# Kernel tuning notes

Hardware: AMD Instinct MI355X
Metric: run time of the kernel (lower is better)

The kernel has to match this reference:

```python
import jax, jax.numpy as jnp
import numpy as np

N, D = 16384, 16     # nodes (hits), node feature dim (= embedding dim, slice is full)
K = 64               # max_num_neighbors
MAX_RADIUS = 6.0     # kNN radius cut
PID_MAX = 5000


def setup_inputs() -> dict:
    key = jax.random.key(0)
    k1, k2 = jax.random.split(key)
    x = jax.random.normal(k1, (N, D), dtype=jnp.float32)
    particle_id = jax.random.randint(k2, (N,), 0, PID_MAX, dtype=jnp.int32)
    return {"x": x, "particle_id": particle_id}


def reference(x, particle_id):
    # ml is None and embedding_slice=(None,None) -> embedding features are x itself
    emb = x
    # knn_graph: squared pairwise distances, self-loops excluded (diag = +inf)
    sq = jnp.sum(emb * emb, axis=1)                       # [N]
    d2 = sq[:, None] + sq[None, :] - 2.0 * (emb @ emb.T)  # [N, N]
    diag = jnp.arange(N)
    d2 = d2.at[diag, diag].set(jnp.inf)
    _, nbr = jax.lax.top_k(-d2, K)                        # [N, K] nearest neighbor ids
    src = nbr.reshape(-1)                                 # edge_index[0]: neighbor (source)
    dst = jnp.repeat(jnp.arange(N, dtype=src.dtype), K)   # edge_index[1]: query node
    # radius filter: keep edges with dist < max_radius (fixed shape -> boolean mask)
    diff = x[src] - x[dst]                                # [N*K, D]
    dists = jnp.sqrt(jnp.maximum(jnp.sum(diff * diff, axis=1), 0.0))
    mask = dists < MAX_RADIUS                             # [N*K]
    # edge truth labels: same (nonzero) particle id on both ends
    y = (particle_id[src] == particle_id[dst]) & (particle_id[src] > 0) & mask
    # edge features: [x_src - x_dst, x_src + x_dst], zeroed on masked-out edges
    edge_features = jnp.concatenate([diff, x[src] + x[dst]], axis=1)
    edge_features = edge_features * mask[:, None].astype(x.dtype)
    edge_index = jnp.stack([src, dst])                    # [2, N*K]
    return x, edge_index, y.astype(jnp.int32), edge_features, mask
```

## Files before the change

kernel.cpp:

```cpp
#include <hip/hip_runtime.h>
#include <hip/hip_fp16.h>

#define NN 16384
#define DD 16
#define KK 64
#define QQ 4
#define TPB 256
#define NQW 16
#define HIST 1024
#define HISTW (HIST/2)
#define LIST_MAX 768
#define CAND_MAX 256
#define EPS 1.5f

__device__ __forceinline__ float halving_sumsq16(const float* v) {
    float p[16];
#pragma unroll
    for (int d = 0; d < 16; ++d) p[d] = __fmul_rn(v[d], v[d]);
    float r8[8];
#pragma unroll
    for (int j = 0; j < 8; ++j) r8[j] = __fadd_rn(p[j], p[j + 8]);
    float r4[4];
#pragma unroll
    for (int j = 0; j < 4; ++j) r4[j] = __fadd_rn(r8[j], r8[j + 4]);
    float r2[2];
#pragma unroll
    for (int j = 0; j < 2; ++j) r2[j] = __fadd_rn(r4[j], r4[j + 2]);
    return __fadd_rn(r2[0], r2[1]);
}

__device__ __forceinline__ float d2_of(const float* xi, const float* xj,
                                       float sqi, float sqj) {
    float dot = 0.0f;
#pragma unroll
    for (int d = 0; d < DD; ++d) dot = fmaf(xi[d], xj[d], dot);
    return __fsub_rn(__fadd_rn(sqi, sqj), __fmul_rn(2.0f, dot));
}

__device__ __forceinline__ int bucket_of(float d2) {
    int b = (int)__fmul_rn(d2, 4.0f);
    if (b < 0) b = 0;
    if (b >= HIST) b = HIST - 1;
    return b;
}

__device__ __forceinline__ float tq_of(float s) {
    return 16.0f + s - 2.0f * sqrtf(32.0f + 4.0f * s);
}

#define LOAD_XQ()                                                              \
    float xq[QQ][DD];                                                          \
    float sq[QQ], Tq[QQ];                                                      \
    _Pragma("unroll") for (int q = 0; q < QQ; ++q) {                           \
        const float4* p = reinterpret_cast<const float4*>(x + (iA + q) * DD);  \
        float4 a0 = p[0], a1 = p[1], a2 = p[2], a3 = p[3];                     \
        xq[q][0]=a0.x; xq[q][1]=a0.y; xq[q][2]=a0.z; xq[q][3]=a0.w;            \
        xq[q][4]=a1.x; xq[q][5]=a1.y; xq[q][6]=a1.z; xq[q][7]=a1.w;            \
        xq[q][8]=a2.x; xq[q][9]=a2.y; xq[q][10]=a2.z; xq[q][11]=a2.w;          \
        xq[q][12]=a3.x; xq[q][13]=a3.y; xq[q][14]=a3.z; xq[q][15]=a3.w;        \
        sq[q] = sqf[iA + q];                                                   \
        Tq[q] = tq_of(sq[q]);                                                  \
    }

#define LOAD_XJ(j)                                                             \
    const float4* xj4 = reinterpret_cast<const float4*>(x + (j) * DD);         \
    float4 a0 = xj4[0], a1 = xj4[1], a2 = xj4[2], a3 = xj4[3];                 \
    float xj[DD] = {a0.x, a0.y, a0.z, a0.w, a1.x, a1.y, a1.z, a1.w,            \
                    a2.x, a2.y, a2.z, a2.w, a3.x, a3.y, a3.z, a3.w};

__global__ void prep_kernel(const float* __restrict__ x,
                            float* __restrict__ out_x,
                            float* __restrict__ sqf,
                            __half* __restrict__ xh) {
    int i = blockIdx.x * blockDim.x + threadIdx.x;
    if (i < NN) {
        float v[DD];
#pragma unroll
        for (int d = 0; d < DD; ++d) v[d] = x[i * DD + d];
        sqf[i] = halving_sumsq16(v);
#pragma unroll
        for (int p = 0; p < 8; ++p) {
            xh[((long)p * NN + i) * 2 + 0] = __float2half(v[2 * p]);
            xh[((long)p * NN + i) * 2 + 1] = __float2half(v[2 * p + 1]);
        }
    }
    for (int t = i; t < NN * DD; t += gridDim.x * blockDim.x) {
        out_x[t] = x[t];
    }
}

__global__ __launch_bounds__(TPB, 4) void scan_kernel(
        const __half2* __restrict__ xh2,
        const float* __restrict__ sqf,
        unsigned int* __restrict__ ws_cnt,
        unsigned short* __restrict__ ws_list) {
    __shared__ unsigned short bm[NQW][TPB];
    __shared__ unsigned short list[QQ][LIST_MAX];
    __shared__ unsigned int wcnt[TPB / 64][QQ];
    __shared__ unsigned int s_listcnt[QQ];

    const int tid = threadIdx.x;
    const int lane = tid & 63;
    const int w = tid >> 6;
    const int iA = blockIdx.x * QQ;

    __half2 qh[QQ][8];
    float Cq[QQ];
#pragma unroll
    for (int q = 0; q < QQ; ++q) {
        const float* xr = (const float*)sqf;
    }
#pragma unroll
    for (int q = 0; q < QQ; ++q)
#pragma unroll
        for (int p = 0; p < 8; ++p)
            qh[q][p] = xh2[(long)p * NN + (iA + q)];
#pragma unroll
    for (int q = 0; q < QQ; ++q) {
        float s = sqf[iA + q];
        Cq[q] = 0.5f * (s - tq_of(s) - EPS);
    }

#pragma unroll 1
    for (int c = 0; c < NQW; ++c) {
        const int qd = c * TPB + tid;
        float4 sjv = reinterpret_cast<const float4*>(sqf)[qd];
        __half2 acc[QQ][4];
#pragma unroll
        for (int q = 0; q < QQ; ++q)
#pragma unroll
            for (int jl = 0; jl < 4; ++jl)
                acc[q][jl] = __half2(__float2half(0.f), __float2half(0.f));
#pragma unroll
        for (int p = 0; p < 8; ++p) {
            const __half2* hp = &xh2[(long)p * NN + 4 * (long)qd];
            __half2 h0 = hp[0], h1 = hp[1], h2 = hp[2], h3 = hp[3];
#pragma unroll
            for (int q = 0; q < QQ; ++q) {
                acc[q][0] = __hfma2(qh[q][p], h0, acc[q][0]);
                acc[q][1] = __hfma2(qh[q][p], h1, acc[q][1]);
                acc[q][2] = __hfma2(qh[q][p], h2, acc[q][2]);
                acc[q][3] = __hfma2(qh[q][p], h3, acc[q][3]);
            }
        }
        unsigned int bits = 0;
        float sjq[4] = {sjv.x, sjv.y, sjv.z, sjv.w};
#pragma unroll
        for (int jl = 0; jl < 4; ++jl) {
#pragma unroll
            for (int q = 0; q < QQ; ++q) {
                float dot = __low2float(acc[q][jl]) + __high2float(acc[q][jl]);
                float thr = fmaf(sjq[jl], 0.5f, Cq[q]);
                if (dot > thr) bits |= (1u << (jl * 4 + q));
            }
        }
        bm[c][tid] = (unsigned short)bits;
    }
    __syncthreads();

    {
        unsigned int cnt[QQ] = {0, 0, 0, 0};
#pragma unroll 1
        for (int c = 0; c < NQW; ++c) {
            unsigned int w16 = bm[c][tid];
#pragma unroll
            for (int q = 0; q < QQ; ++q)
                cnt[q] += (unsigned int)__popc(w16 & (0x1111u << q));
        }
        unsigned int excl[QQ];
#pragma unroll
        for (int q = 0; q < QQ; ++q) {
            unsigned int v = cnt[q];
#pragma unroll
            for (int off = 1; off < 64; off <<= 1) {
                unsigned int n = __shfl_up(v, off, 64);
                if (lane >= off) v += n;
            }
            excl[q] = v - cnt[q];
            if (lane == 63) wcnt[w][q] = v;
        }
        __syncthreads();
        if (tid < QQ)
            s_listcnt[tid] = wcnt[0][tid] + wcnt[1][tid] + wcnt[2][tid] + wcnt[3][tid];
        unsigned int cur[QQ];
#pragma unroll
        for (int q = 0; q < QQ; ++q) {
            unsigned int b = 0;
            for (int ww = 0; ww < w; ++ww) b += wcnt[ww][q];
            cur[q] = b + excl[q];
        }
#pragma unroll 1
        for (int c = 0; c < NQW; ++c) {
            unsigned int t16 = bm[c][tid];
            while (t16) {
                int b = __ffs(t16) - 1;
                int q = b & 3;
                int jl = b >> 2;
                unsigned int pos = cur[q]++;
                if (pos < LIST_MAX)
                    list[q][pos] = (unsigned short)((c * TPB + tid) * 4 + jl);
                t16 &= t16 - 1;
            }
        }
    }
    __syncthreads();

    for (int q = 0; q < QQ; ++q) {
        int lc = (int)min(s_listcnt[q], (unsigned int)LIST_MAX);
        unsigned short* dst = ws_list + ((long)iA + q) * LIST_MAX;
        for (int e = tid; e < lc; e += TPB) dst[e] = list[q][e];
    }
    if (tid < QQ) ws_cnt[iA + tid] = s_listcnt[tid];
}

__global__ __launch_bounds__(TPB) void select_kernel(
        const float* __restrict__ x,
        const int* __restrict__ pid,
        const float* __restrict__ sqf,
        const unsigned int* __restrict__ ws_cnt,
        const unsigned short* __restrict__ ws_list,
        float* __restrict__ out_src,
        float* __restrict__ out_dst,
        float* __restrict__ out_y,
        float* __restrict__ out_ef,
        float* __restrict__ out_mask) {
    __shared__ unsigned short list[QQ][LIST_MAX];
    __shared__ unsigned int hist[QQ][HISTW];
    __shared__ unsigned int cand_key[QQ][CAND_MAX];
    __shared__ int cand_idx[QQ][CAND_MAX];
    __shared__ unsigned int wavesum[QQ][TPB / 64];
    __shared__ int s_bsel[QQ];
    __shared__ unsigned int s_excnt[QQ], s_candcnt[QQ], s_lc[QQ];
    __shared__ int s_fb[QQ];

    const int bid = blockIdx.x;
    const int tid = threadIdx.x;
    const int lane = tid & 63;
    const int w = tid >> 6;
    const int iA = bid * QQ;

    for (int t = tid; t < QQ * HISTW; t += TPB)
        ((unsigned int*)hist)[t] = 0;
    if (tid < QQ) {
        s_excnt[tid] = 0; s_candcnt[tid] = 0; s_bsel[tid] = HIST - 1;
        s_lc[tid] = min(ws_cnt[iA + tid], (unsigned int)LIST_MAX);
    }
    LOAD_XQ();
    __syncthreads();

    for (int q = 0; q < QQ; ++q) {
        const unsigned short* src = ws_list + ((long)iA + q) * LIST_MAX;
        const int lc = (int)s_lc[q];
        for (int e = tid; e < lc; e += TPB) list[q][e] = src[e];
    }
    __syncthreads();

    for (int q = 0; q < QQ; ++q) {
        const int lc = (int)s_lc[q];
        unsigned int my = 0;
        for (int e = tid; e < lc; e += TPB) {
            const int j = list[q][e];
            LOAD_XJ(j);
            float d2 = d2_of(xq[q], xj, sq[q], sqf[j]);
            my += (d2 < Tq[q]) ? 1u : 0u;
            int b = bucket_of(d2);
            atomicAdd(&hist[q][b >> 1], 1u << ((b & 1) << 4));
        }
        unsigned int v = my;
#pragma unroll
        for (int off = 1; off < 64; off <<= 1) v += __shfl_xor(v, off, 64);
        if (lane == 0 && v) atomicAdd(&s_excnt[q], v);
    }
    __syncthreads();

    if (tid < QQ)
        s_fb[tid] = (ws_cnt[iA + tid] > LIST_MAX) || (s_excnt[tid] < KK + 1);
    __syncthreads();
    const int anyfb = s_fb[0] | s_fb[1] | s_fb[2] | s_fb[3];

    if (anyfb) {
#pragma unroll
        for (int q = 0; q < QQ; ++q)
            if (s_fb[q])
                for (int t = tid; t < HISTW; t += TPB) hist[q][t] = 0;
        __syncthreads();
        for (int j = tid; j < NN; j += TPB) {
            LOAD_XJ(j);
            const float sj = sqf[j];
#pragma unroll
            for (int q = 0; q < QQ; ++q) {
                if (s_fb[q] && j != iA + q) {
                    float d2 = d2_of(xq[q], xj, sq[q], sj);
                    int b = bucket_of(d2);
                    atomicAdd(&hist[q][b >> 1], 1u << ((b & 1) << 4));
                }
            }
        }
    }
    __syncthreads();

    {
        unsigned int local[QQ], inc[QQ];
        unsigned int pc0[QQ], pc1[QQ], pc2[QQ], pc3[QQ];
#pragma unroll
        for (int q = 0; q < QQ; ++q) {
            unsigned int h0 = hist[q][2 * tid];
            unsigned int h1 = hist[q][2 * tid + 1];
            pc0[q] = h0 & 0xFFFFu; pc1[q] = h0 >> 16;
            pc2[q] = h1 & 0xFFFFu; pc3[q] = h1 >> 16;
            unsigned int s = pc0[q] + pc1[q] + pc2[q] + pc3[q];
            local[q] = s;
            unsigned int v = s;
#pragma unroll
            for (int off = 1; off < 64; off <<= 1) {
                unsigned int n = __shfl_up(v, off, 64);
                if (lane >= off) v += n;
            }
            inc[q] = v;
        }
        if (lane == 63)
#pragma unroll
            for (int q = 0; q < QQ; ++q) wavesum[q][w] = inc[q];
        __syncthreads();
#pragma unroll
        for (int q = 0; q < QQ; ++q) {
            const unsigned int need = s_fb[q] ? KK : (KK + 1);
            unsigned int woff = 0;
            for (int ww = 0; ww < w; ++ww) woff += wavesum[q][ww];
            unsigned int cum = inc[q] + woff;
            unsigned int prev = cum - local[q];
            if (prev < need && need <= cum) {
                unsigned int acc = prev;
                int b = 4 * tid;
                if (acc + pc0[q] < need) { acc += pc0[q]; ++b;
                    if (acc + pc1[q] < need) { acc += pc1[q]; ++b;
                        if (acc + pc2[q] < need) { acc += pc2[q]; ++b; } } }
                s_bsel[q] = b;
            }
        }
    }
    __syncthreads();

#pragma unroll
    for (int q = 0; q < QQ; ++q) {
        if (!s_fb[q]) {
            const int bsel = s_bsel[q];
            const int lc = (int)s_lc[q];
            for (int e = tid; e < lc; e += TPB) {
                const int j = list[q][e];
                LOAD_XJ(j);
                float d2 = d2_of(xq[q], xj, sq[q], sqf[j]);
                if (bucket_of(d2) <= bsel && j != iA + q) {
                    unsigned int pos = atomicAdd(&s_candcnt[q], 1u);
                    if (pos < CAND_MAX) {
                        unsigned int u = __float_as_uint(d2);
                        u ^= (u & 0x80000000u) ? 0xFFFFFFFFu : 0x80000000u;
                        cand_key[q][pos] = u;
                        cand_idx[q][pos] = j;
                    }
                }
            }
        }
    }
    if (anyfb) {
        for (int j = tid; j < NN; j += TPB) {
            LOAD_XJ(j);
            const float sj = sqf[j];
#pragma unroll
            for (int q = 0; q < QQ; ++q) {
                if (s_fb[q] && j != iA + q) {
                    float d2 = d2_of(xq[q], xj, sq[q], sj);
                    if (bucket_of(d2) <= s_bsel[q]) {
                        unsigned int pos = atomicAdd(&s_candcnt[q], 1u);
                        if (pos < CAND_MAX) {
                            unsigned int u = __float_as_uint(d2);
                            u ^= (u & 0x80000000u) ? 0xFFFFFFFFu : 0x80000000u;
                            cand_key[q][pos] = u;
                            cand_idx[q][pos] = j;
                        }
                    }
                }
            }
        }
    }
    __syncthreads();

    for (int q = 0; q < QQ; ++q) {
        const int iq = iA + q;
        const int mypid = pid[iq];
        int c = (int)s_candcnt[q];
        if (c > CAND_MAX) c = CAND_MAX;
        for (int t = tid; t < c; t += TPB) {
            const unsigned int kt = cand_key[q][t];
            const int jt = cand_idx[q][t];
            int rank = 0;
            for (int u = 0; u < c; ++u) {
                unsigned int ku = cand_key[q][u];
                rank += (ku < kt) || (ku == kt && cand_idx[q][u] < jt);
            }
            if (rank < KK) {
                const long e = (long)iq * KK + rank;
                out_src[e] = (float)jt;

                const float* xjp = x + jt * DD;
                float diff[DD], sum[DD];
#pragma unroll
                for (int d = 0; d < DD; ++d) {
                    float a = xjp[d], b = xq[q][d];
                    diff[d] = __fsub_rn(a, b);
                    sum[d]  = __fadd_rn(a, b);
                }
                const float s2 = halving_sumsq16(diff);
                const bool m = __fsqrt_rn(s2) < 6.0f;
                out_mask[e] = m ? 1.0f : 0.0f;
                const int pj = pid[jt];
                out_y[e] = (m && pj == mypid && pj > 0) ? 1.0f : 0.0f;

                float* ef = out_ef + e * (2 * DD);
#pragma unroll
                for (int d = 0; d < DD; ++d) ef[d] = m ? diff[d] : 0.0f;
#pragma unroll
                for (int d = 0; d < DD; ++d) ef[DD + d] = m ? sum[d] : 0.0f;
            }
        }
    }

    for (int t = tid; t < QQ * KK; t += TPB) {
        out_dst[(long)iA * KK + t] = (float)(iA + t / KK);
    }
}

extern "C" void kernel_launch(void* const* d_in, const int* in_sizes, int n_in,
                              void* d_out, int out_size, void* d_ws, size_t ws_size,
                              hipStream_t stream) {
    const float* x = (const float*)d_in[0];
    const int* pid = (const int*)d_in[1];
    float* out = (float*)d_out;

    float* out_x   = out;
    float* out_src = out_x + NN * DD;
    float* out_dst = out_src + NN * KK;
    float* out_y   = out_dst + NN * KK;
    float* out_ef  = out_y + NN * KK;
    float* out_mask = out_ef + (long)NN * KK * 2 * DD;

    char* wsb = (char*)d_ws;
    float* sqf = (float*)wsb;
    __half* xh = (__half*)(wsb + (long)NN * 4);
    unsigned int* ws_cnt =
        (unsigned int*)(wsb + (long)NN * 4 + (long)NN * DD * 2);
    unsigned short* ws_list =
        (unsigned short*)(wsb + (long)NN * 4 + (long)NN * DD * 2 + (long)NN * 4);

    prep_kernel<<<NN / 256, 256, 0, stream>>>(x, out_x, sqf, xh);
    scan_kernel<<<NN / QQ, TPB, 0, stream>>>((const __half2*)xh, sqf,
                                             ws_cnt, ws_list);
    select_kernel<<<NN / QQ, TPB, 0, stream>>>(x, pid, sqf, ws_cnt, ws_list,
                                               out_src, out_dst, out_y,
                                               out_ef, out_mask);
}
```

Baseline: 418.9 us.

## Emit quantized approximate distances from scan and histogram them without recomputation

```diff
diff --git a/kernel.cpp b/kernel.cpp
--- a/kernel.cpp
+++ b/kernel.cpp
@@ -12,6 +12,7 @@
 #define LIST_MAX 768
 #define CAND_MAX 256
 #define EPS 1.5f
+#define EB 10
 
 __device__ __forceinline__ float halving_sumsq16(const float* v) {
     float p[16];
@@ -93,33 +94,25 @@
         const __half2* __restrict__ xh2,
         const float* __restrict__ sqf,
         unsigned int* __restrict__ ws_cnt,
-        unsigned short* __restrict__ ws_list) {
-    __shared__ unsigned short bm[NQW][TPB];
-    __shared__ unsigned short list[QQ][LIST_MAX];
-    __shared__ unsigned int wcnt[TPB / 64][QQ];
-    __shared__ unsigned int s_listcnt[QQ];
+        unsigned int* __restrict__ ws_list) {
+    __shared__ unsigned int s_cnt[QQ];
 
     const int tid = threadIdx.x;
-    const int lane = tid & 63;
-    const int w = tid >> 6;
     const int iA = blockIdx.x * QQ;
 
+    if (tid < QQ) s_cnt[tid] = 0;
+
     __half2 qh[QQ][8];
-    float Cq[QQ];
+    float sqv[QQ], Cq[QQ];
 #pragma unroll
     for (int q = 0; q < QQ; ++q) {
-        const float* xr = (const float*)sqf;
-    }
-#pragma unroll
-    for (int q = 0; q < QQ; ++q)
-#pragma unroll
-        for (int p = 0; p < 8; ++p)
-            qh[q][p] = xh2[(long)p * NN + (iA + q)];
-#pragma unroll
-    for (int q = 0; q < QQ; ++q) {
+#pragma unroll
+        for (int p = 0; p < 8; ++p) qh[q][p] = xh2[(long)p * NN + (iA + q)];
         float s = sqf[iA + q];
+        sqv[q] = s;
         Cq[q] = 0.5f * (s - tq_of(s) - EPS);
     }
+    __syncthreads();
 
 #pragma unroll 1
     for (int c = 0; c < NQW; ++c) {
@@ -143,74 +136,27 @@
                 acc[q][3] = __hfma2(qh[q][p], h3, acc[q][3]);
             }
         }
-        unsigned int bits = 0;
         float sjq[4] = {sjv.x, sjv.y, sjv.z, sjv.w};
 #pragma unroll
         for (int jl = 0; jl < 4; ++jl) {
 #pragma unroll
             for (int q = 0; q < QQ; ++q) {
                 float dot = __low2float(acc[q][jl]) + __high2float(acc[q][jl]);
-                float thr = fmaf(sjq[jl], 0.5f, Cq[q]);
-                if (dot > thr) bits |= (1u << (jl * 4 + q));
-            }
-        }
-        bm[c][tid] = (unsigned short)bits;
-    }
-    __syncthreads();
-
-    {
-        unsigned int cnt[QQ] = {0, 0, 0, 0};
-#pragma unroll 1
-        for (int c = 0; c < NQW; ++c) {
-            unsigned int w16 = bm[c][tid];
-#pragma unroll
-            for (int q = 0; q < QQ; ++q)
-                cnt[q] += (unsigned int)__popc(w16 & (0x1111u << q));
-        }
-        unsigned int excl[QQ];
-#pragma unroll
-        for (int q = 0; q < QQ; ++q) {
-            unsigned int v = cnt[q];
-#pragma unroll
-            for (int off = 1; off < 64; off <<= 1) {
-                unsigned int n = __shfl_up(v, off, 64);
-                if (lane >= off) v += n;
-            }
-            excl[q] = v - cnt[q];
-            if (lane == 63) wcnt[w][q] = v;
-        }
-        __syncthreads();
-        if (tid < QQ)
-            s_listcnt[tid] = wcnt[0][tid] + wcnt[1][tid] + wcnt[2][tid] + wcnt[3][tid];
-        unsigned int cur[QQ];
-#pragma unroll
-        for (int q = 0; q < QQ; ++q) {
-            unsigned int b = 0;
-            for (int ww = 0; ww < w; ++ww) b += wcnt[ww][q];
-            cur[q] = b + excl[q];
-        }
-#pragma unroll 1
-        for (int c = 0; c < NQW; ++c) {
-            unsigned int t16 = bm[c][tid];
-            while (t16) {
-                int b = __ffs(t16) - 1;
-                int q = b & 3;
-                int jl = b >> 2;
-                unsigned int pos = cur[q]++;
-                if (pos < LIST_MAX)
-                    list[q][pos] = (unsigned short)((c * TPB + tid) * 4 + jl);
-                t16 &= t16 - 1;
-            }
-        }
-    }
-    __syncthreads();
-
-    for (int q = 0; q < QQ; ++q) {
-        int lc = (int)min(s_listcnt[q], (unsigned int)LIST_MAX);
-        unsigned short* dst = ws_list + ((long)iA + q) * LIST_MAX;
-        for (int e = tid; e < lc; e += TPB) dst[e] = list[q][e];
-    }
-    if (tid < QQ) ws_cnt[iA + tid] = s_listcnt[tid];
+                if (dot > fmaf(sjq[jl], 0.5f, Cq[q])) {
+                    float d2a = (sqv[q] + sjq[jl]) - 2.0f * dot;
+                    int qd2 = (int)__fmul_rn(d2a, 256.0f);
+                    qd2 = qd2 < 0 ? 0 : (qd2 > 65535 ? 65535 : qd2);
+                    unsigned int pos = atomicAdd(&s_cnt[q], 1u);
+                    if (pos < LIST_MAX)
+                        ws_list[(long)(iA + q) * LIST_MAX + pos] =
+                            ((unsigned int)qd2 << 16) |
+                            (unsigned int)(4 * qd + jl);
+                }
+            }
+        }
+    }
+    __syncthreads();
+    if (tid < QQ) ws_cnt[iA + tid] = s_cnt[tid];
 }
 
 __global__ __launch_bounds__(TPB) void select_kernel(
@@ -218,19 +164,19 @@
         const int* __restrict__ pid,
         const float* __restrict__ sqf,
         const unsigned int* __restrict__ ws_cnt,
-        const unsigned short* __restrict__ ws_list,
+        const unsigned int* __restrict__ ws_list,
         float* __restrict__ out_src,
         float* __restrict__ out_dst,
         float* __restrict__ out_y,
         float* __restrict__ out_ef,
         float* __restrict__ out_mask) {
-    __shared__ unsigned short list[QQ][LIST_MAX];
+    __shared__ unsigned int list32[QQ][LIST_MAX];
     __shared__ unsigned int hist[QQ][HISTW];
     __shared__ unsigned int cand_key[QQ][CAND_MAX];
     __shared__ int cand_idx[QQ][CAND_MAX];
     __shared__ unsigned int wavesum[QQ][TPB / 64];
     __shared__ int s_bsel[QQ];
-    __shared__ unsigned int s_excnt[QQ], s_candcnt[QQ], s_lc[QQ];
+    __shared__ unsigned int s_lowcnt[QQ], s_candcnt[QQ], s_lc[QQ];
     __shared__ int s_fb[QQ];
 
     const int bid = blockIdx.x;
@@ -242,60 +188,28 @@
     for (int t = tid; t < QQ * HISTW; t += TPB)
         ((unsigned int*)hist)[t] = 0;
     if (tid < QQ) {
-        s_excnt[tid] = 0; s_candcnt[tid] = 0; s_bsel[tid] = HIST - 1;
+        s_lowcnt[tid] = 0; s_candcnt[tid] = 0; s_bsel[tid] = -1;
         s_lc[tid] = min(ws_cnt[iA + tid], (unsigned int)LIST_MAX);
     }
     LOAD_XQ();
     __syncthreads();
 
     for (int q = 0; q < QQ; ++q) {
-        const unsigned short* src = ws_list + ((long)iA + q) * LIST_MAX;
+        const unsigned int* src = ws_list + (long)(iA + q) * LIST_MAX;
         const int lc = (int)s_lc[q];
-        for (int e = tid; e < lc; e += TPB) list[q][e] = src[e];
-    }
-    __syncthreads();
-
-    for (int q = 0; q < QQ; ++q) {
-        const int lc = (int)s_lc[q];
+        const int lthr = (int)__fmul_rn(Tq[q] - EPS, 256.0f) - 2;
         unsigned int my = 0;
         for (int e = tid; e < lc; e += TPB) {
-            const int j = list[q][e];
-            LOAD_XJ(j);
-            float d2 = d2_of(xq[q], xj, sq[q], sqf[j]);
-            my += (d2 < Tq[q]) ? 1u : 0u;
-            int b = bucket_of(d2);
+            unsigned int ent = src[e];
+            list32[q][e] = ent;
+            int b = (int)(ent >> 22);
             atomicAdd(&hist[q][b >> 1], 1u << ((b & 1) << 4));
+            my += ((int)(ent >> 16) < lthr) ? 1u : 0u;
         }
         unsigned int v = my;
 #pragma unroll
         for (int off = 1; off < 64; off <<= 1) v += __shfl_xor(v, off, 64);
-        if (lane == 0 && v) atomicAdd(&s_excnt[q], v);
-    }
-    __syncthreads();
-
-    if (tid < QQ)
-        s_fb[tid] = (ws_cnt[iA + tid] > LIST_MAX) || (s_excnt[tid] < KK + 1);
-    __syncthreads();
-    const int anyfb = s_fb[0] | s_fb[1] | s_fb[2] | s_fb[3];
-
-    if (anyfb) {
-#pragma unroll
-        for (int q = 0; q < QQ; ++q)
-            if (s_fb[q])
-                for (int t = tid; t < HISTW; t += TPB) hist[q][t] = 0;
-        __syncthreads();
-        for (int j = tid; j < NN; j += TPB) {
-            LOAD_XJ(j);
-            const float sj = sqf[j];
-#pragma unroll
-            for (int q = 0; q < QQ; ++q) {
-                if (s_fb[q] && j != iA + q) {
-                    float d2 = d2_of(xq[q], xj, sq[q], sj);
-                    int b = bucket_of(d2);
-                    atomicAdd(&hist[q][b >> 1], 1u << ((b & 1) << 4));
-                }
-            }
-        }
+        if (lane == 0 && v) atomicAdd(&s_lowcnt[q], v);
     }
     __syncthreads();
 
@@ -324,45 +238,115 @@
         __syncthreads();
 #pragma unroll
         for (int q = 0; q < QQ; ++q) {
-            const unsigned int need = s_fb[q] ? KK : (KK + 1);
             unsigned int woff = 0;
             for (int ww = 0; ww < w; ++ww) woff += wavesum[q][ww];
             unsigned int cum = inc[q] + woff;
             unsigned int prev = cum - local[q];
-            if (prev < need && need <= cum) {
+            if (prev < KK + 1 && KK + 1 <= cum) {
                 unsigned int acc = prev;
                 int b = 4 * tid;
-                if (acc + pc0[q] < need) { acc += pc0[q]; ++b;
-                    if (acc + pc1[q] < need) { acc += pc1[q]; ++b;
-                        if (acc + pc2[q] < need) { acc += pc2[q]; ++b; } } }
+                if (acc + pc0[q] < KK + 1) { acc += pc0[q]; ++b;
+                    if (acc + pc1[q] < KK + 1) { acc += pc1[q]; ++b;
+                        if (acc + pc2[q] < KK + 1) { acc += pc2[q]; ++b; } } }
                 s_bsel[q] = b;
             }
         }
     }
     __syncthreads();
 
+    if (tid < QQ)
+        s_fb[tid] = (ws_cnt[iA + tid] > LIST_MAX) ||
+                    (s_lowcnt[tid] < KK + 1) || (s_bsel[tid] < 0);
+    __syncthreads();
+
 #pragma unroll
     for (int q = 0; q < QQ; ++q) {
-        if (!s_fb[q]) {
-            const int bsel = s_bsel[q];
-            const int lc = (int)s_lc[q];
-            for (int e = tid; e < lc; e += TPB) {
-                const int j = list[q][e];
-                LOAD_XJ(j);
-                float d2 = d2_of(xq[q], xj, sq[q], sqf[j]);
-                if (bucket_of(d2) <= bsel && j != iA + q) {
-                    unsigned int pos = atomicAdd(&s_candcnt[q], 1u);
-                    if (pos < CAND_MAX) {
-                        unsigned int u = __float_as_uint(d2);
-                        u ^= (u & 0x80000000u) ? 0xFFFFFFFFu : 0x80000000u;
-                        cand_key[q][pos] = u;
-                        cand_idx[q][pos] = j;
-                    }
-                }
-            }
-        }
-    }
+        if (s_fb[q]) continue;
+        const int cutb = s_bsel[q] + EB;
+        const int lc = (int)s_lc[q];
+        for (int e = tid; e < lc; e += TPB) {
+            const unsigned int ent = list32[q][e];
+            if ((int)(ent >> 22) <= cutb) {
+                const int j = (int)(ent & 0xFFFFu);
+                if (j == iA + q) continue;
+                unsigned int pos = atomicAdd(&s_candcnt[q], 1u);
+                if (pos < CAND_MAX) {
+                    LOAD_XJ(j);
+                    float d2 = d2_of(xq[q], xj, sq[q], sqf[j]);
+                    unsigned int u = __float_as_uint(d2);
+                    u ^= (u & 0x80000000u) ? 0xFFFFFFFFu : 0x80000000u;
+                    cand_key[q][pos] = u;
+                    cand_idx[q][pos] = j;
+                }
+            }
+        }
+    }
+    __syncthreads();
+    if (tid < QQ && s_candcnt[tid] > CAND_MAX) s_fb[tid] = 1;
+    __syncthreads();
+    const int anyfb = s_fb[0] | s_fb[1] | s_fb[2] | s_fb[3];
+
     if (anyfb) {
+        if (tid < QQ && s_fb[tid]) { s_candcnt[tid] = 0; s_bsel[tid] = HIST - 1; }
+#pragma unroll
+        for (int q = 0; q < QQ; ++q)
+            if (s_fb[q])
+                for (int t = tid; t < HISTW; t += TPB) hist[q][t] = 0;
+        __syncthreads();
+        for (int j = tid; j < NN; j += TPB) {
+            LOAD_XJ(j);
+            const float sj = sqf[j];
+#pragma unroll
+            for (int q = 0; q < QQ; ++q) {
+                if (s_fb[q] && j != iA + q) {
+                    float d2 = d2_of(xq[q], xj, sq[q], sj);
+                    int b = bucket_of(d2);
+                    atomicAdd(&hist[q][b >> 1], 1u << ((b & 1) << 4));
+                }
+            }
+        }
+        __syncthreads();
+        {
+            unsigned int local[QQ], inc[QQ];
+            unsigned int pc0[QQ], pc1[QQ], pc2[QQ], pc3[QQ];
+#pragma unroll
+            for (int q = 0; q < QQ; ++q) {
+                unsigned int h0 = hist[q][2 * tid];
+                unsigned int h1 = hist[q][2 * tid + 1];
+                pc0[q] = h0 & 0xFFFFu; pc1[q] = h0 >> 16;
+                pc2[q] = h1 & 0xFFFFu; pc3[q] = h1 >> 16;
+                unsigned int s = pc0[q] + pc1[q] + pc2[q] + pc3[q];
+                local[q] = s;
+                unsigned int v = s;
+#pragma unroll
+                for (int off = 1; off < 64; off <<= 1) {
+                    unsigned int n = __shfl_up(v, off, 64);
+                    if (lane >= off) v += n;
+                }
+                inc[q] = v;
+            }
+            if (lane == 63)
+#pragma unroll
+                for (int q = 0; q < QQ; ++q) wavesum[q][w] = inc[q];
+            __syncthreads();
+#pragma unroll
+            for (int q = 0; q < QQ; ++q) {
+                if (!s_fb[q]) continue;
+                unsigned int woff = 0;
+                for (int ww = 0; ww < w; ++ww) woff += wavesum[q][ww];
+                unsigned int cum = inc[q] + woff;
+                unsigned int prev = cum - local[q];
+                if (prev < KK && KK <= cum) {
+                    unsigned int acc = prev;
+                    int b = 4 * tid;
+                    if (acc + pc0[q] < KK) { acc += pc0[q]; ++b;
+                        if (acc + pc1[q] < KK) { acc += pc1[q]; ++b;
+                            if (acc + pc2[q] < KK) { acc += pc2[q]; ++b; } } }
+                    s_bsel[q] = b;
+                }
+            }
+        }
+        __syncthreads();
         for (int j = tid; j < NN; j += TPB) {
             LOAD_XJ(j);
             const float sj = sqf[j];
@@ -449,8 +433,8 @@
     __half* xh = (__half*)(wsb + (long)NN * 4);
     unsigned int* ws_cnt =
         (unsigned int*)(wsb + (long)NN * 4 + (long)NN * DD * 2);
-    unsigned short* ws_list =
-        (unsigned short*)(wsb + (long)NN * 4 + (long)NN * DD * 2 + (long)NN * 4);
+    unsigned int* ws_list =
+        (unsigned int*)(wsb + (long)NN * 4 + (long)NN * DD * 2 + (long)NN * 4);
 
     prep_kernel<<<NN / 256, 256, 0, stream>>>(x, out_x, sqf, xh);
     scan_kernel<<<NN / QQ, TPB, 0, stream>>>((const __half2*)xh, sqf,
```

Result: slower. 784.8 us (+87.4%).
